# Optimization experiments

Hardware: AMD Instinct MI355X
Metric: run time of the kernel (lower is better)

Reference implementation:

```python
import jax, jax.numpy as jnp
import numpy as np

# Elman RNN (SRNN). Dropout is treated as identity (eval/inference mode),
# since the reference baseline must be deterministic.

def setup_inputs() -> dict:
    key = jax.random.key(0)
    k1, k2, k3, k4 = jax.random.split(key, 4)
    B, S, I, H = 32, 2048, 256, 256
    x = jax.random.normal(k1, (B, S, I), dtype=jnp.float32)
    Wx_w = jax.random.normal(k2, (H, I), dtype=jnp.float32) * (1.0 / np.sqrt(I))
    Wx_b = jax.random.normal(k3, (H,), dtype=jnp.float32) * 0.01
    Wh_w = jax.random.normal(k4, (H, H), dtype=jnp.float32) * (1.0 / np.sqrt(H))
    return {"x": x, "Wx_w": Wx_w, "Wx_b": Wx_b, "Wh_w": Wh_w}


def reference(x, Wx_w, Wx_b, Wh_w):
    B, S, I = x.shape
    H = Wx_w.shape[0]
    # Precompute input projection for all timesteps in one batched GEMM: [B,S,H]
    xw = jnp.einsum('bsi,hi->bsh', x, Wx_w) + Wx_b
    xw_t = jnp.swapaxes(xw, 0, 1)  # [S,B,H] for scan over time

    def step(h, xw_step):
        h_new = jnp.tanh(xw_step + h @ Wh_w.T)  # [B,H]
        return h_new, h_new

    h0 = jnp.zeros((B, H), dtype=x.dtype)
    h_last, outs = jax.lax.scan(step, h0, xw_t)  # outs: [S,B,H]
    outputs = jnp.swapaxes(outs, 0, 1)  # [B,S,H]
    return outputs, h_last
```

## Files before the change

### kernel.cpp

```cpp
#include <hip/hip_runtime.h>

#define B 32
#define S 2048
#define I 256
#define H 256

#define NWORK  64
#define NRNN   32
#define NTILE  1024
#define NFLAG  512
#define PFD    8

typedef _Float16 h2 __attribute__((ext_vector_type(2)));
typedef float    f4 __attribute__((ext_vector_type(4)));

__device__ __forceinline__ float fdot2(h2 a, h2 b, float c) {
#if __has_builtin(__builtin_amdgcn_fdot2)
    return __builtin_amdgcn_fdot2(a, b, c, false);
#else
    return fmaf((float)a[1], (float)b[1], fmaf((float)a[0], (float)b[0], c));
#endif
}

__device__ __forceinline__ void nt_store4(float* p, float4 v) {
    __builtin_nontemporal_store(__builtin_bit_cast(f4, v), (f4*)p);
}

__device__ __forceinline__ void lds_barrier() {
    __asm__ __volatile__("" ::: "memory");
    __builtin_amdgcn_s_waitcnt(0xC07F);
    __builtin_amdgcn_s_barrier();
    __asm__ __volatile__("" ::: "memory");
}

__device__ __forceinline__ float fast_tanh(float x) {
#if __has_builtin(__builtin_amdgcn_exp2f) && __has_builtin(__builtin_amdgcn_rcpf)
    float e = __builtin_amdgcn_exp2f(x * 2.8853900818f);
    float r = __builtin_amdgcn_rcpf(e + 1.0f);
    return fmaf(-2.0f, r, 1.0f);
#else
    float e = __expf(2.0f * x);
    return 1.0f - __fdividef(2.0f, e + 1.0f);
#endif
}

__device__ __forceinline__ float dpp_xor1(float x) {
    return __builtin_bit_cast(float, __builtin_amdgcn_mov_dpp(
        __builtin_bit_cast(int, x), 0xB1, 0xF, 0xF, false));
}
__device__ __forceinline__ float dpp_xor2(float x) {
    return __builtin_bit_cast(float, __builtin_amdgcn_mov_dpp(
        __builtin_bit_cast(int, x), 0x4E, 0xF, 0xF, false));
}

__device__ __forceinline__ void wait_flag(const int* f) {
    long long t0 = __builtin_amdgcn_s_memrealtime();
    while (__hip_atomic_load(f, __ATOMIC_ACQUIRE, __HIP_MEMORY_SCOPE_AGENT) != 2) {
        __builtin_amdgcn_s_sleep(8);
        if (__builtin_amdgcn_s_memrealtime() - t0 > 25000000LL) break;
    }
}

__global__ void zero_flags(int* flags) { flags[threadIdx.x] = 0; }

#define TM 128
#define TN 128
#define TK 32
#define LDP (TM + 4)

__device__ __forceinline__ void gemm_tile(
    const float* __restrict__ x, const float* __restrict__ Wxw,
    const float* __restrict__ Wxb, float* __restrict__ out,
    float (*As)[LDP], float (*Bs)[LDP], int t, int m0, int n0)
{
    const int lr = t >> 3;
    const int lc = t & 7;
    const int tn = t & 15, tm = t >> 4;

    float acc[8][8] = {};
    float bias[8];
#pragma unroll
    for (int jj = 0; jj < 4; ++jj) {
        bias[jj]     = Wxb[n0 + 4 * tn + jj];
        bias[4 + jj] = Wxb[n0 + 64 + 4 * tn + jj];
    }

    float4 va[4], vb[4];
#pragma unroll
    for (int hh = 0; hh < 4; ++hh) {
        const int m = lr + 32 * hh;
        va[hh] = *(const float4*)(x   + (size_t)(m0 + m) * I + 4 * lc);
        vb[hh] = *(const float4*)(Wxw + (size_t)(n0 + m) * I + 4 * lc);
    }

    for (int kt = 0; kt < I; kt += TK) {
#pragma unroll
        for (int hh = 0; hh < 4; ++hh) {
            const int m = lr + 32 * hh;
            float4 v = va[hh];
            As[4 * lc + 0][m] = v.x; As[4 * lc + 1][m] = v.y;
            As[4 * lc + 2][m] = v.z; As[4 * lc + 3][m] = v.w;
            float4 wv = vb[hh];
            Bs[4 * lc + 0][m] = wv.x; Bs[4 * lc + 1][m] = wv.y;
            Bs[4 * lc + 2][m] = wv.z; Bs[4 * lc + 3][m] = wv.w;
        }
        lds_barrier();
        if (kt + TK < I) {
#pragma unroll
            for (int hh = 0; hh < 4; ++hh) {
                const int m = lr + 32 * hh;
                va[hh] = *(const float4*)(x   + (size_t)(m0 + m) * I + kt + TK + 4 * lc);
                vb[hh] = *(const float4*)(Wxw + (size_t)(n0 + m) * I + kt + TK + 4 * lc);
            }
        }
#pragma unroll
        for (int k = 0; k < TK; ++k) {
            float4 a0 = *(const float4*)&As[k][4 * tm];
            float4 a1 = *(const float4*)&As[k][4 * tm + 64];
            float4 b0 = *(const float4*)&Bs[k][4 * tn];
            float4 b1 = *(const float4*)&Bs[k][4 * tn + 64];
            float av[8] = {a0.x, a0.y, a0.z, a0.w, a1.x, a1.y, a1.z, a1.w};
            float bv[8] = {b0.x, b0.y, b0.z, b0.w, b1.x, b1.y, b1.z, b1.w};
#pragma unroll
            for (int i2 = 0; i2 < 8; ++i2)
#pragma unroll
                for (int jj = 0; jj < 8; ++jj)
                    acc[i2][jj] = fmaf(av[i2], bv[jj], acc[i2][jj]);
        }
        lds_barrier();
    }
#pragma unroll
    for (int hi = 0; hi < 2; ++hi) {
#pragma unroll
        for (int i2 = 0; i2 < 4; ++i2) {
            const int r = m0 + 64 * hi + 4 * tm + i2;
            float4 v0 = { acc[4 * hi + i2][0] + bias[0], acc[4 * hi + i2][1] + bias[1],
                          acc[4 * hi + i2][2] + bias[2], acc[4 * hi + i2][3] + bias[3] };
            float4 v1 = { acc[4 * hi + i2][4] + bias[4], acc[4 * hi + i2][5] + bias[5],
                          acc[4 * hi + i2][6] + bias[6], acc[4 * hi + i2][7] + bias[7] };
            nt_store4(out + (size_t)r * H + n0 + 4 * tn,      v0);
            nt_store4(out + (size_t)r * H + n0 + 64 + 4 * tn, v1);
        }
    }
}

__device__ __forceinline__ void rnn_body(
    const float* __restrict__ Whw, float* __restrict__ out,
    _Float16 (*hsh)[4][72], int b, int t, const int* flags)
{
    const int w = t >> 6;
    const int l = t & 63;
    const int j = l >> 2;
    const int q = l & 3;

    h2 wreg[4][32];
#pragma unroll
    for (int i = 0; i < 4; ++i) {
        const float4* wp =
            (const float4*)(Whw + (size_t)(64 * w + 4 * j + (q ^ i)) * H + 64 * q);
#pragma unroll
        for (int m = 0; m < 16; ++m) {
            float4 f = wp[m];
            wreg[i][2 * m]     = h2{(_Float16)f.x, (_Float16)f.y};
            wreg[i][2 * m + 1] = h2{(_Float16)f.z, (_Float16)f.w};
        }
    }
#pragma unroll
    for (int i = 0; i < 4; ++i)
#pragma unroll
        for (int m = 0; m < 32; ++m) {
            unsigned tmp = __builtin_bit_cast(unsigned, wreg[i][m]);
            __asm__("" : "+v"(tmp));
            wreg[i][m] = __builtin_bit_cast(h2, tmp);
        }

    hsh[0][w][l] = (_Float16)0.0f;
    __syncthreads();

    if (flags) {
        if (t == 0) wait_flag(flags + 0);
        __syncthreads();
    }

    float* outb = out + (size_t)b * S * H + t;
    float* op = outb;

    float xr[PFD];
#pragma unroll
    for (int i = 0; i < PFD; ++i) xr[i] = outb[(size_t)i * H];
    const float* lp = outb + (size_t)PFD * H;

    float hv = 0.f;
    for (int c = 0; c < 16; ++c) {
#pragma unroll 8
        for (int sl = 0; sl < 128; ++sl) {
            const int p  = sl & 1;
            const int rp = sl & (PFD - 1);
            if (sl == 120 && c < 15 && flags) {
                if (t == 0) wait_flag(flags + c + 1);
                __syncthreads();
            }
            float xw0 = xr[rp];

            const uint4* hp = (const uint4*)&hsh[p][q][0];
            float acc0 = 0.f, acc1 = 0.f, acc2 = 0.f, acc3 = 0.f;
#pragma unroll
            for (int u = 0; u < 8; ++u) {
                uint4 v = hp[u];
                h2 q0 = __builtin_bit_cast(h2, v.x);
                h2 q1 = __builtin_bit_cast(h2, v.y);
                h2 q2 = __builtin_bit_cast(h2, v.z);
                h2 q3 = __builtin_bit_cast(h2, v.w);
                acc0 = fdot2(wreg[0][4 * u + 0], q0, acc0);
                acc0 = fdot2(wreg[0][4 * u + 1], q1, acc0);
                acc0 = fdot2(wreg[0][4 * u + 2], q2, acc0);
                acc0 = fdot2(wreg[0][4 * u + 3], q3, acc0);
                acc1 = fdot2(wreg[1][4 * u + 0], q0, acc1);
                acc1 = fdot2(wreg[1][4 * u + 1], q1, acc1);
                acc1 = fdot2(wreg[1][4 * u + 2], q2, acc1);
                acc1 = fdot2(wreg[1][4 * u + 3], q3, acc1);
                acc2 = fdot2(wreg[2][4 * u + 0], q0, acc2);
                acc2 = fdot2(wreg[2][4 * u + 1], q1, acc2);
                acc2 = fdot2(wreg[2][4 * u + 2], q2, acc2);
                acc2 = fdot2(wreg[2][4 * u + 3], q3, acc2);
                acc3 = fdot2(wreg[3][4 * u + 0], q0, acc3);
                acc3 = fdot2(wreg[3][4 * u + 1], q1, acc3);
                acc3 = fdot2(wreg[3][4 * u + 2], q2, acc3);
                acc3 = fdot2(wreg[3][4 * u + 3], q3, acc3);
            }

            float Sa  = acc0 + dpp_xor1(acc1);
            float Sb  = acc2 + dpp_xor1(acc3);
            float sum = Sa + dpp_xor2(Sb);

            hv = fast_tanh(xw0 + sum);
            hsh[p ^ 1][w][l] = (_Float16)hv;
            op[0] = hv;
            op += H;
            xr[rp] = lp[0]; lp += H;

            lds_barrier();
        }
    }
    out[(size_t)B * S * H + (size_t)b * H + t] = hv;
}

__global__ __launch_bounds__(256, 1) void fused_srnn(
    const float* __restrict__ x, const float* __restrict__ Wxw,
    const float* __restrict__ Wxb, const float* __restrict__ Whw,
    float* __restrict__ out, int* __restrict__ flags)
{
    __shared__ __align__(16) float As[TK][LDP];
    __shared__ __align__(16) float Bs[TK][LDP];
    __shared__ __align__(16) _Float16 hsh[2][4][72];

    const int bid = blockIdx.x;
    const int t   = threadIdx.x;

    if (bid < NWORK) {
        for (int tau = bid; tau < NTILE; tau += NWORK) {
            const int st = tau >> 6;
            const int bb = (tau >> 1) & 31;
            const int nt = tau & 1;
            gemm_tile(x, Wxw, Wxb, out, As, Bs, t,
                      bb * S + st * TM, nt * TN);
            __threadfence();
            __syncthreads();
            if (t == 0)
                __hip_atomic_fetch_add(&flags[bb * 16 + st], 1,
                                       __ATOMIC_RELEASE, __HIP_MEMORY_SCOPE_AGENT);
        }
        return;
    }
    rnn_body(Whw, out, hsh, bid - NWORK, t, flags + (bid - NWORK) * 16);
}

__global__ __launch_bounds__(256) void phase1_gemm(
    const float* __restrict__ x, const float* __restrict__ Wxw,
    const float* __restrict__ Wxb, float* __restrict__ out)
{
    __shared__ __align__(16) float As[TK][LDP];
    __shared__ __align__(16) float Bs[TK][LDP];
    gemm_tile(x, Wxw, Wxb, out, As, Bs, threadIdx.x,
              blockIdx.x * TM, blockIdx.y * TN);
}

__global__ __launch_bounds__(256, 1) void phase2_rnn(
    const float* __restrict__ Whw, float* __restrict__ out)
{
    __shared__ __align__(16) _Float16 hsh[2][4][72];
    rnn_body(Whw, out, hsh, blockIdx.x, threadIdx.x, nullptr);
}

extern "C" void kernel_launch(void* const* d_in, const int* in_sizes, int n_in,
                              void* d_out, int out_size, void* d_ws, size_t ws_size,
                              hipStream_t stream) {
    const float* x   = (const float*)d_in[0];
    const float* Wxw = (const float*)d_in[1];
    const float* Wxb = (const float*)d_in[2];
    const float* Whw = (const float*)d_in[3];
    float* out = (float*)d_out;

    if (d_ws != nullptr && ws_size >= NFLAG * sizeof(int)) {
        int* flags = (int*)d_ws;
        zero_flags<<<1, NFLAG, 0, stream>>>(flags);
        fused_srnn<<<NWORK + NRNN, 256, 0, stream>>>(x, Wxw, Wxb, Whw, out, flags);
    } else {
        dim3 g1(B * S / TM, H / TN);
        phase1_gemm<<<g1, 256, 0, stream>>>(x, Wxw, Wxb, out);
        phase2_rnn<<<B, 256, 0, stream>>>(Whw, out);
    }
}
```

Before: 958.0 us.

## Process two batch rows per RNN block to interleave independent recurrences

Each RNN workgroup now runs two independent batch recurrences (A and B) in lockstep, sharing the register-resident recurrent weights and one barrier per step. LDS loads for B are placed between A's MAC blocks so one chain's latency can hide behind the other's arithmetic. The number of RNN blocks drops from 32 to 16. The cost is that each step now does twice the arithmetic on the serial critical path, and register pressure rises.

```diff
diff --git a/kernel.cpp b/kernel.cpp
--- a/kernel.cpp
+++ b/kernel.cpp
@@ -6,7 +6,7 @@
 #define H 256
 
 #define NWORK  64
-#define NRNN   32
+#define NRNN   16
 #define NTILE  1024
 #define NFLAG  512
 #define PFD    8
@@ -144,9 +144,33 @@
     }
 }
 
-__device__ __forceinline__ void rnn_body(
+#define MAC16(A0,A1,A2,A3,V,U) do {                                   \
+    h2 c0 = __builtin_bit_cast(h2, (V).x);                            \
+    h2 c1 = __builtin_bit_cast(h2, (V).y);                            \
+    h2 c2 = __builtin_bit_cast(h2, (V).z);                            \
+    h2 c3 = __builtin_bit_cast(h2, (V).w);                            \
+    A0 = fdot2(wreg[0][4*(U)+0], c0, A0);                             \
+    A0 = fdot2(wreg[0][4*(U)+1], c1, A0);                             \
+    A0 = fdot2(wreg[0][4*(U)+2], c2, A0);                             \
+    A0 = fdot2(wreg[0][4*(U)+3], c3, A0);                             \
+    A1 = fdot2(wreg[1][4*(U)+0], c0, A1);                             \
+    A1 = fdot2(wreg[1][4*(U)+1], c1, A1);                             \
+    A1 = fdot2(wreg[1][4*(U)+2], c2, A1);                             \
+    A1 = fdot2(wreg[1][4*(U)+3], c3, A1);                             \
+    A2 = fdot2(wreg[2][4*(U)+0], c0, A2);                             \
+    A2 = fdot2(wreg[2][4*(U)+1], c1, A2);                             \
+    A2 = fdot2(wreg[2][4*(U)+2], c2, A2);                             \
+    A2 = fdot2(wreg[2][4*(U)+3], c3, A2);                             \
+    A3 = fdot2(wreg[3][4*(U)+0], c0, A3);                             \
+    A3 = fdot2(wreg[3][4*(U)+1], c1, A3);                             \
+    A3 = fdot2(wreg[3][4*(U)+2], c2, A3);                             \
+    A3 = fdot2(wreg[3][4*(U)+3], c3, A3);                             \
+} while (0)
+
+__device__ __forceinline__ void rnn_body2(
     const float* __restrict__ Whw, float* __restrict__ out,
-    _Float16 (*hsh)[4][72], int b, int t, const int* flags)
+    _Float16 (*hshA)[4][72], _Float16 (*hshB)[4][72],
+    int bA, int bB, int t, const int* flagsA, const int* flagsB)
 {
     const int w = t >> 6;
     const int l = t & 63;
@@ -174,75 +198,85 @@
             wreg[i][m] = __builtin_bit_cast(h2, tmp);
         }
 
-    hsh[0][w][l] = (_Float16)0.0f;
+    hshA[0][w][l] = (_Float16)0.0f;
+    hshB[0][w][l] = (_Float16)0.0f;
     __syncthreads();
 
-    if (flags) {
-        if (t == 0) wait_flag(flags + 0);
+    if (flagsA) {
+        if (t == 0) { wait_flag(flagsA + 0); wait_flag(flagsB + 0); }
         __syncthreads();
     }
 
-    float* outb = out + (size_t)b * S * H + t;
-    float* op = outb;
-
-    float xr[PFD];
-#pragma unroll
-    for (int i = 0; i < PFD; ++i) xr[i] = outb[(size_t)i * H];
-    const float* lp = outb + (size_t)PFD * H;
-
-    float hv = 0.f;
+    float* outbA = out + (size_t)bA * S * H + t;
+    float* outbB = out + (size_t)bB * S * H + t;
+    float *opA = outbA, *opB = outbB;
+
+    float xrA[PFD], xrB[PFD];
+#pragma unroll
+    for (int i = 0; i < PFD; ++i) {
+        xrA[i] = outbA[(size_t)i * H];
+        xrB[i] = outbB[(size_t)i * H];
+    }
+    const float* lpA = outbA + (size_t)PFD * H;
+    const float* lpB = outbB + (size_t)PFD * H;
+
+    float hvA = 0.f, hvB = 0.f;
     for (int c = 0; c < 16; ++c) {
 #pragma unroll 8
         for (int sl = 0; sl < 128; ++sl) {
             const int p  = sl & 1;
             const int rp = sl & (PFD - 1);
-            if (sl == 120 && c < 15 && flags) {
-                if (t == 0) wait_flag(flags + c + 1);
+            if (sl == 120 && c < 15 && flagsA) {
+                if (t == 0) { wait_flag(flagsA + c + 1); wait_flag(flagsB + c + 1); }
                 __syncthreads();
             }
-            float xw0 = xr[rp];
-
-            const uint4* hp = (const uint4*)&hsh[p][q][0];
-            float acc0 = 0.f, acc1 = 0.f, acc2 = 0.f, acc3 = 0.f;
-#pragma unroll
-            for (int u = 0; u < 8; ++u) {
-                uint4 v = hp[u];
-                h2 q0 = __builtin_bit_cast(h2, v.x);
-                h2 q1 = __builtin_bit_cast(h2, v.y);
-                h2 q2 = __builtin_bit_cast(h2, v.z);
-                h2 q3 = __builtin_bit_cast(h2, v.w);
-                acc0 = fdot2(wreg[0][4 * u + 0], q0, acc0);
-                acc0 = fdot2(wreg[0][4 * u + 1], q1, acc0);
-                acc0 = fdot2(wreg[0][4 * u + 2], q2, acc0);
-                acc0 = fdot2(wreg[0][4 * u + 3], q3, acc0);
-                acc1 = fdot2(wreg[1][4 * u + 0], q0, acc1);
-                acc1 = fdot2(wreg[1][4 * u + 1], q1, acc1);
-                acc1 = fdot2(wreg[1][4 * u + 2], q2, acc1);
-                acc1 = fdot2(wreg[1][4 * u + 3], q3, acc1);
-                acc2 = fdot2(wreg[2][4 * u + 0], q0, acc2);
-                acc2 = fdot2(wreg[2][4 * u + 1], q1, acc2);
-                acc2 = fdot2(wreg[2][4 * u + 2], q2, acc2);
-                acc2 = fdot2(wreg[2][4 * u + 3], q3, acc2);
-                acc3 = fdot2(wreg[3][4 * u + 0], q0, acc3);
-                acc3 = fdot2(wreg[3][4 * u + 1], q1, acc3);
-                acc3 = fdot2(wreg[3][4 * u + 2], q2, acc3);
-                acc3 = fdot2(wreg[3][4 * u + 3], q3, acc3);
-            }
-
-            float Sa  = acc0 + dpp_xor1(acc1);
-            float Sb  = acc2 + dpp_xor1(acc3);
-            float sum = Sa + dpp_xor2(Sb);
-
-            hv = fast_tanh(xw0 + sum);
-            hsh[p ^ 1][w][l] = (_Float16)hv;
-            op[0] = hv;
-            op += H;
-            xr[rp] = lp[0]; lp += H;
+            const uint4* hpA = (const uint4*)&hshA[p][q][0];
+            const uint4* hpB = (const uint4*)&hshB[p][q][0];
+
+            uint4 vA[8];
+#pragma unroll
+            for (int u = 0; u < 8; ++u) vA[u] = hpA[u];
+            float xwA = xrA[rp], xwB = xrB[rp];
+            xrA[rp] = lpA[0]; lpA += H;
+            xrB[rp] = lpB[0]; lpB += H;
+
+            float aA0 = 0.f, aA1 = 0.f, aA2 = 0.f, aA3 = 0.f;
+#pragma unroll
+            for (int u = 0; u < 4; ++u) MAC16(aA0, aA1, aA2, aA3, vA[u], u);
+            uint4 vB0[4];
+#pragma unroll
+            for (int u = 0; u < 4; ++u) vB0[u] = hpB[u];
+#pragma unroll
+            for (int u = 4; u < 8; ++u) MAC16(aA0, aA1, aA2, aA3, vA[u], u);
+            uint4 vB1[4];
+#pragma unroll
+            for (int u = 0; u < 4; ++u) vB1[u] = hpB[u + 4];
+
+            float SaA  = aA0 + dpp_xor1(aA1);
+            float SbA  = aA2 + dpp_xor1(aA3);
+            float sumA = SaA + dpp_xor2(SbA);
+            hvA = fast_tanh(xwA + sumA);
+            hshA[p ^ 1][w][l] = (_Float16)hvA;
+            opA[0] = hvA; opA += H;
+
+            float aB0 = 0.f, aB1 = 0.f, aB2 = 0.f, aB3 = 0.f;
+#pragma unroll
+            for (int u = 0; u < 4; ++u) MAC16(aB0, aB1, aB2, aB3, vB0[u], u);
+#pragma unroll
+            for (int u = 4; u < 8; ++u) MAC16(aB0, aB1, aB2, aB3, vB1[u - 4], u);
+
+            float SaB  = aB0 + dpp_xor1(aB1);
+            float SbB  = aB2 + dpp_xor1(aB3);
+            float sumB = SaB + dpp_xor2(SbB);
+            hvB = fast_tanh(xwB + sumB);
+            hshB[p ^ 1][w][l] = (_Float16)hvB;
+            opB[0] = hvB; opB += H;
 
             lds_barrier();
         }
     }
-    out[(size_t)B * S * H + (size_t)b * H + t] = hv;
+    out[(size_t)B * S * H + (size_t)bA * H + t] = hvA;
+    out[(size_t)B * S * H + (size_t)bB * H + t] = hvB;
 }
 
 __global__ __launch_bounds__(256, 1) void fused_srnn(
@@ -252,7 +286,8 @@
 {
     __shared__ __align__(16) float As[TK][LDP];
     __shared__ __align__(16) float Bs[TK][LDP];
-    __shared__ __align__(16) _Float16 hsh[2][4][72];
+    __shared__ __align__(16) _Float16 hshA[2][4][72];
+    __shared__ __align__(16) _Float16 hshB[2][4][72];
 
     const int bid = blockIdx.x;
     const int t   = threadIdx.x;
@@ -272,7 +307,9 @@
         }
         return;
     }
-    rnn_body(Whw, out, hsh, bid - NWORK, t, flags + (bid - NWORK) * 16);
+    const int r = bid - NWORK;
+    rnn_body2(Whw, out, hshA, hshB, 2 * r, 2 * r + 1, t,
+              flags + (2 * r) * 16, flags + (2 * r + 1) * 16);
 }
 
 __global__ __launch_bounds__(256) void phase1_gemm(
@@ -288,8 +325,11 @@
 __global__ __launch_bounds__(256, 1) void phase2_rnn(
     const float* __restrict__ Whw, float* __restrict__ out)
 {
-    __shared__ __align__(16) _Float16 hsh[2][4][72];
-    rnn_body(Whw, out, hsh, blockIdx.x, threadIdx.x, nullptr);
+    __shared__ __align__(16) _Float16 hshA[2][4][72];
+    __shared__ __align__(16) _Float16 hshB[2][4][72];
+    const int r = blockIdx.x;
+    rnn_body2(Whw, out, hshA, hshB, 2 * r, 2 * r + 1, threadIdx.x,
+              nullptr, nullptr);
 }
 
 extern "C" void kernel_launch(void* const* d_in, const int* in_sizes, int n_in,
@@ -308,6 +348,6 @@
     } else {
         dim3 g1(B * S / TM, H / TN);
         phase1_gemm<<<g1, 256, 0, stream>>>(x, Wxw, Wxb, out);
-        phase2_rnn<<<B, 256, 0, stream>>>(Whw, out);
-    }
-}
+        phase2_rnn<<<NRNN, 256, 0, stream>>>(Whw, out);
+    }
+}
```

Measured after the change: 1.615 ms. +68.6%, slower.
